# Optimization experiments

Measured on AMD Instinct MI355X. Metric: run time of the kernel, lower is better.

## Reference

```python
import jax, jax.numpy as jnp
import numpy as np

B, S, I, H = 64, 512, 512, 1024


def setup_inputs() -> dict:
    key = jax.random.key(0)
    ks = jax.random.split(key, 5)
    bound = 1.0 / np.sqrt(H)  # nn.GRUCell default init
    u = lambda k, shape: jax.random.uniform(k, shape, jnp.float32, -bound, bound)
    return {
        "input": jax.random.normal(ks[0], (B, S, I), jnp.float32),
        "state": jnp.zeros((B, H), jnp.float32),
        "weight_ih": u(ks[1], (3 * H, I)),
        "weight_hh": u(ks[2], (3 * H, H)),
        "bias_ih": u(ks[3], (3 * H,)),
        "bias_hh": u(ks[4], (3 * H,)),
        "gamma_ih": jnp.ones((3 * H,), jnp.float32),
        "gamma_hh": jnp.ones((3 * H,), jnp.float32),
    }


def _ln_x(x, g, b):
    # kefirski's _layer_norm_x: (x - mean) / std (unbiased std, eps=0)
    mean = jnp.mean(x, axis=-1, keepdims=True)
    std = jnp.std(x, axis=-1, keepdims=True, ddof=1)
    return g * ((x - mean) / std) + b


def _ln_h(x, g, b):
    # kefirski's _layer_norm_h: mean-subtraction only
    return g * (x - jnp.mean(x, axis=-1, keepdims=True)) + b


def reference(input, state, weight_ih, weight_hh, bias_ih, bias_hh, gamma_ih, gamma_hh):
    Hd = state.shape[-1]
    # Input-side projections + LN are h-independent -> precompute over all timesteps
    ih = jnp.einsum("bsi,gi->bsg", input, weight_ih)  # [B,S,3H]
    ih_rz = _ln_x(ih[..., : 2 * Hd], gamma_ih[: 2 * Hd], bias_ih[: 2 * Hd])  # [B,S,2H]
    ih_n = _ln_x(ih[..., 2 * Hd :], gamma_ih[2 * Hd :], bias_ih[2 * Hd :])  # [B,S,H]

    def step(h, xs):
        irz, inn = xs  # [B,2H], [B,H]
        hh = h @ weight_hh.T  # [B,3H]
        hh_rz = _ln_h(hh[:, : 2 * Hd], gamma_hh[: 2 * Hd], bias_hh[: 2 * Hd])
        hh_n = _ln_h(hh[:, 2 * Hd :], gamma_hh[2 * Hd :], bias_hh[2 * Hd :])
        rz = jax.nn.sigmoid(irz + hh_rz)
        r, z = rz[:, :Hd], rz[:, Hd:]
        n = jnp.tanh(inn + r * hh_n)
        h_new = (1.0 - z) * n + z * h
        return h_new, h_new

    final_state, outs = jax.lax.scan(
        step, state, (ih_rz.transpose(1, 0, 2), ih_n.transpose(1, 0, 2))
    )
    return outs.transpose(1, 0, 2), final_state  # [B,S,H], [B,H]
```

## Files before the change

### kernel.cpp

```cpp
#include <hip/hip_runtime.h>
#include <stdint.h>
#include <stddef.h>

#define B_  64
#define S_  512
#define I_  512
#define H_  1024
#define G_  3072
#define NWG 64
#define CPW 32

typedef short short8 __attribute__((ext_vector_type(8)));
typedef float f32x4  __attribute__((ext_vector_type(4)));
typedef unsigned short u16x4 __attribute__((ext_vector_type(4)));

__device__ __forceinline__ unsigned short f32_to_bf16(float f){
  unsigned u = __builtin_bit_cast(unsigned, f);
  u = (u + 0x7FFFu + ((u >> 16) & 1u)) >> 16;
  return (unsigned short)u;
}
__device__ __forceinline__ float bf16_to_f32(unsigned short s){
  unsigned u = ((unsigned)s) << 16;
  return __builtin_bit_cast(float, u);
}
__device__ __forceinline__ float sig_(float x){ return 1.0f/(1.0f + __expf(-x)); }
__device__ __forceinline__ float tanh_(float x){
  float ax = fabsf(x);
  float t = __expf(-2.0f*ax);
  float r = (1.0f - t)/(1.0f + t);
  return copysignf(r, x);
}

__device__ __forceinline__ short8 ldg16_coh(const unsigned short* p){
  short8 r;
  asm volatile("global_load_dwordx4 %0, %1, off sc0 sc1" : "=v"(r) : "v"(p) : "memory");
  return r;
}
__device__ __forceinline__ void stg8_coh(unsigned short* p, u16x4 v){
  asm volatile("global_store_dwordx2 %0, %1, off sc0 sc1" :: "v"(p), "v"(v) : "memory");
}
__device__ __forceinline__ void stg4_coh(unsigned* p, unsigned v){
  asm volatile("global_store_dword %0, %1, off sc0 sc1" :: "v"(p), "v"(v) : "memory");
}
__device__ __forceinline__ unsigned ldg4_coh_wait(const unsigned* p){
  unsigned r;
  asm volatile("global_load_dword %0, %1, off sc0 sc1\n\ts_waitcnt vmcnt(0)"
               : "=v"(r) : "v"(p) : "memory");
  return r;
}
__device__ __forceinline__ u16x4 ldg8(const unsigned short* p){
  u16x4 r;
  asm volatile("global_load_dwordx2 %0, %1, off" : "=v"(r) : "v"(p) : "memory");
  return r;
}

__global__ __launch_bounds__(256) void k_cvt4(const float* __restrict__ src,
                                              unsigned short* __restrict__ dst, int n4){
  int i = blockIdx.x*blockDim.x + threadIdx.x;
  int st = gridDim.x*blockDim.x;
  for (; i < n4; i += st){
    f32x4 v = *(const f32x4*)(src + (size_t)i*4);
    u16x4 o;
    o[0]=f32_to_bf16(v[0]); o[1]=f32_to_bf16(v[1]);
    o[2]=f32_to_bf16(v[2]); o[3]=f32_to_bf16(v[3]);
    *(u16x4*)(dst + (size_t)i*4) = o;
  }
}

__global__ __launch_bounds__(256) void k_cmean(const float* __restrict__ whh,
                                               unsigned short* __restrict__ CM){
  int k = blockIdx.x*256 + threadIdx.x;
  float s0 = 0.f, s1 = 0.f;
  for (int j = 0; j < 2048; ++j) s0 += whh[(size_t)j*H_ + k];
  for (int j = 2048; j < 3072; ++j) s1 += whh[(size_t)j*H_ + k];
  CM[k]      = f32_to_bf16(s0 * (1.0f/2048.0f));
  CM[H_ + k] = f32_to_bf16(s1 * (1.0f/1024.0f));
  for (int r = 2; r < 16; ++r) CM[(size_t)r*H_ + k] = 0;
}

__global__ __launch_bounds__(256, 2) void k_gemm_ih(
    const unsigned short* __restrict__ X,
    const unsigned short* __restrict__ W,
    unsigned short* __restrict__ IH)
{
  __shared__ __align__(16) short As[128*32];
  __shared__ __align__(16) short Bs[128*32];
  int bid = blockIdx.x;
  int mt = bid / 24, nt = bid % 24;
  int tid = threadIdx.x, lane = tid & 63, wid = tid >> 6;
  int vr = wid >> 1, vc = wid & 1;
  int r0s = tid >> 2, r1s = r0s + 64;
  int sc = (tid & 3) * 8;
  const unsigned short* xa0 = X + (size_t)(mt*128 + r0s)*512 + sc;
  const unsigned short* xa1 = X + (size_t)(mt*128 + r1s)*512 + sc;
  const unsigned short* wb0 = W + (size_t)(nt*128 + r0s)*512 + sc;
  const unsigned short* wb1 = W + (size_t)(nt*128 + r1s)*512 + sc;

  f32x4 acc[4][4];
  #pragma unroll
  for (int m=0;m<4;m++)
    #pragma unroll
    for (int n=0;n<4;n++) acc[m][n] = (f32x4){0.f,0.f,0.f,0.f};

  short8 ra0 = *(const short8*)xa0;
  short8 ra1 = *(const short8*)xa1;
  short8 rb0 = *(const short8*)wb0;
  short8 rb1 = *(const short8*)wb1;
  int ko = (lane >> 4) * 8;

  for (int kt = 0; kt < 16; ++kt){
    __syncthreads();
    *(short8*)&As[r0s*32 + sc] = ra0;
    *(short8*)&As[r1s*32 + sc] = ra1;
    *(short8*)&Bs[r0s*32 + sc] = rb0;
    *(short8*)&Bs[r1s*32 + sc] = rb1;
    __syncthreads();
    if (kt < 15){
      ra0 = *(const short8*)(xa0 + (kt+1)*32);
      ra1 = *(const short8*)(xa1 + (kt+1)*32);
      rb0 = *(const short8*)(wb0 + (kt+1)*32);
      rb1 = *(const short8*)(wb1 + (kt+1)*32);
    }
    short8 af[4], bfr[4];
    #pragma unroll
    for (int m=0;m<4;m++) af[m]  = *(const short8*)&As[(vr*64 + m*16 + (lane&15))*32 + ko];
    #pragma unroll
    for (int n=0;n<4;n++) bfr[n] = *(const short8*)&Bs[(vc*64 + n*16 + (lane&15))*32 + ko];
    #pragma unroll
    for (int m=0;m<4;m++)
      #pragma unroll
      for (int n=0;n<4;n++)
        acc[m][n] = __builtin_amdgcn_mfma_f32_16x16x32_bf16(af[m], bfr[n], acc[m][n], 0,0,0);
  }
  int row0 = mt*128 + vr*64, col0 = nt*128 + vc*64;
  int rl = (lane >> 4) * 4, cl = lane & 15;
  #pragma unroll
  for (int m=0;m<4;m++)
    #pragma unroll
    for (int n=0;n<4;n++)
      #pragma unroll
      for (int r=0;r<4;r++){
        int row = row0 + m*16 + rl + r;
        int rowT = ((row & 511) << 6) | (row >> 9);
        IH[(size_t)rowT*G_ + (col0 + n*16 + cl)] = f32_to_bf16(acc[m][n][r]);
      }
}

__global__ __launch_bounds__(256) void k_ln(
    unsigned short* __restrict__ IH,
    const float* __restrict__ gih,
    const float* __restrict__ bih)
{
  __shared__ float red[4][4];
  int row = blockIdx.x, tid = threadIdx.x, lane = tid & 63, wid = tid >> 6;
  unsigned short* p = IH + (size_t)row * G_;
  float xv[3][4];
  #pragma unroll
  for (int q=0;q<3;q++){
    u16x4 v = *(const u16x4*)(p + (tid + q*256)*4);
    #pragma unroll
    for (int j=0;j<4;j++) xv[q][j] = bf16_to_f32(v[j]);
  }
  float s0=0, q0=0, s1=0, q1=0;
  #pragma unroll
  for (int q=0;q<2;q++)
    #pragma unroll
    for (int j=0;j<4;j++){ s0 += xv[q][j]; q0 += xv[q][j]*xv[q][j]; }
  #pragma unroll
  for (int j=0;j<4;j++){ s1 += xv[2][j]; q1 += xv[2][j]*xv[2][j]; }
  #pragma unroll
  for (int off=32; off>0; off>>=1){
    s0 += __shfl_down(s0, off, 64);
    q0 += __shfl_down(q0, off, 64);
    s1 += __shfl_down(s1, off, 64);
    q1 += __shfl_down(q1, off, 64);
  }
  if (lane == 0){ red[wid][0]=s0; red[wid][1]=q0; red[wid][2]=s1; red[wid][3]=q1; }
  __syncthreads();
  float S0 = red[0][0]+red[1][0]+red[2][0]+red[3][0];
  float Q0 = red[0][1]+red[1][1]+red[2][1]+red[3][1];
  float S1 = red[0][2]+red[1][2]+red[2][2]+red[3][2];
  float Q1 = red[0][3]+red[1][3]+red[2][3]+red[3][3];
  float m0 = S0 * (1.0f/2048.0f);
  float rs0 = rsqrtf(fmaxf((Q0 - S0*m0) * (1.0f/2047.0f), 1e-20f));
  float m1 = S1 * (1.0f/1024.0f);
  float rs1 = rsqrtf(fmaxf((Q1 - S1*m1) * (1.0f/1023.0f), 1e-20f));
  #pragma unroll
  for (int q=0;q<3;q++){
    int base = (tid + q*256)*4;
    u16x4 o;
    #pragma unroll
    for (int j=0;j<4;j++){
      int col = base + j;
      float y = (q<2) ? (xv[q][j]-m0)*rs0 : (xv[q][j]-m1)*rs1;
      o[j] = f32_to_bf16(gih[col]*y + bih[col]);
    }
    *(u16x4*)(p + base) = o;
  }
}

__global__ __launch_bounds__(256, 1) void k_gru(
    const unsigned short* __restrict__ IH,
    const unsigned short* __restrict__ WHH,
    const unsigned short* __restrict__ CM,
    unsigned short* __restrict__ HB,
    const float* __restrict__ ghh,
    const float* __restrict__ bhh,
    const float* __restrict__ state,
    float* __restrict__ out,
    unsigned* __restrict__ FLAGS)
{
  __shared__ float PSUM[4][112][34];
  const int g = blockIdx.x & 31;
  const int p = blockIdx.x >> 5;
  const int tid = threadIdx.x;
  const int lane = tid & 63;
  const int wv = tid >> 6;
  const int l15 = lane & 15;
  const int lho = (lane >> 4) << 3;
  const int colbase = g * CPW;
  const int rowbase = p * 32;

  short8 bfr[7][8];
  #pragma unroll
  for (int ct = 0; ct < 7; ++ct){
    const unsigned short* src = (ct < 6)
        ? (WHH + (size_t)((ct>>1)*H_ + colbase + (ct&1)*16 + l15)*H_)
        : (CM + (size_t)l15*H_);
    #pragma unroll
    for (int ks = 0; ks < 8; ++ks)
      bfr[ct][ks] = *(const short8*)(src + wv*256 + ks*32 + lho);
  }

  const int b_ = tid & 31;
  const int cq = tid >> 5;
  const int c0 = colbase + cq*4;
  const int gb = rowbase + b_;
  float gr[4],gz[4],gn[4],br_[4],bz_[4],bn_[4],hv[4];
  #pragma unroll
  for (int j = 0; j < 4; ++j){
    gr[j] = ghh[c0+j];   gz[j] = ghh[H_+c0+j];   gn[j] = ghh[2*H_+c0+j];
    br_[j]= bhh[c0+j];   bz_[j]= bhh[H_+c0+j];   bn_[j]= bhh[2*H_+c0+j];
    hv[j] = state[(size_t)gb*H_ + c0 + j];
  }

  const unsigned* myflag = FLAGS + (p*32 + (lane & 31))*16;
  int cur = 0;

  for (int t = 0; t < S_; ++t){
    const unsigned short* ihp = IH + ((size_t)t*B_ + gb)*G_;
    u16x4 ir  = ldg8(ihp + c0);
    u16x4 izv = ldg8(ihp + H_ + c0);
    u16x4 inv = ldg8(ihp + 2*H_ + c0);

    for (;;){
      unsigned v = ldg4_coh_wait(myflag);
      if (__all((int)(v >= (unsigned)t))) break;
    }

    const unsigned short* hb = HB + cur*(B_*H_);
    short8 af[8][2];
    #pragma unroll
    for (int ks = 0; ks < 8; ++ks)
      #pragma unroll
      for (int rt = 0; rt < 2; ++rt)
        af[ks][rt] = ldg16_coh(hb + (size_t)(rowbase + rt*16 + l15)*H_ + wv*256 + ks*32 + lho);

    f32x4 acc[7][2];
    #pragma unroll
    for (int ct = 0; ct < 7; ++ct)
      #pragma unroll
      for (int rt = 0; rt < 2; ++rt)
        acc[ct][rt] = (f32x4){0.f,0.f,0.f,0.f};

    #pragma unroll
    for (int ks = 0; ks < 8; ++ks){
      asm volatile("s_waitcnt vmcnt(%0)" :: "i"(14 - 2*ks) : "memory");
      __builtin_amdgcn_sched_barrier(0);
      #pragma unroll
      for (int rt = 0; rt < 2; ++rt)
        #pragma unroll
        for (int ct = 0; ct < 7; ++ct)
          acc[ct][rt] = __builtin_amdgcn_mfma_f32_16x16x32_bf16(af[ks][rt], bfr[ct][ks], acc[ct][rt], 0,0,0);
    }

    #pragma unroll
    for (int ct = 0; ct < 7; ++ct)
      #pragma unroll
      for (int rt = 0; rt < 2; ++rt)
        *(f32x4*)&PSUM[wv][ct*16 + l15][rt*16 + (lane>>4)*4] = acc[ct][rt];
    __syncthreads();

    float hhr[4]={0,0,0,0}, hhz[4]={0,0,0,0}, hhn[4]={0,0,0,0};
    float mrz = 0.f, mn = 0.f;
    #pragma unroll
    for (int w = 0; w < 4; ++w){
      #pragma unroll
      for (int j = 0; j < 4; ++j){
        hhr[j] += PSUM[w][cq*4 + j][b_];
        hhz[j] += PSUM[w][32 + cq*4 + j][b_];
        hhn[j] += PSUM[w][64 + cq*4 + j][b_];
      }
      mrz += PSUM[w][96][b_];
      mn  += PSUM[w][97][b_];
    }
    f32x4 ho;
    #pragma unroll
    for (int j = 0; j < 4; ++j){
      float R = sig_(bf16_to_f32(ir[j])  + gr[j]*(hhr[j]-mrz) + br_[j]);
      float Z = sig_(bf16_to_f32(izv[j]) + gz[j]*(hhz[j]-mrz) + bz_[j]);
      float N = tanh_(bf16_to_f32(inv[j]) + R*(gn[j]*(hhn[j]-mn) + bn_[j]));
      hv[j] = (1.0f - Z)*N + Z*hv[j];
      ho[j] = hv[j];
    }
    u16x4 h16;
    #pragma unroll
    for (int j = 0; j < 4; ++j) h16[j] = f32_to_bf16(hv[j]);
    stg8_coh(HB + (cur^1)*(B_*H_) + (size_t)gb*H_ + c0, h16);

    asm volatile("s_waitcnt vmcnt(0)" ::: "memory");
    __syncthreads();
    if (tid == 0) stg4_coh((unsigned*)(FLAGS + (p*32 + g)*16), (unsigned)(t+1));
    *(f32x4*)(out + ((size_t)gb*S_ + t)*H_ + c0) = ho;
    cur ^= 1;
  }
  #pragma unroll
  for (int j = 0; j < 4; ++j)
    out[(size_t)B_*S_*H_ + (size_t)gb*H_ + c0 + j] = hv[j];
}

extern "C" void kernel_launch(void* const* d_in, const int* in_sizes, int n_in,
                              void* d_out, int out_size, void* d_ws, size_t ws_size,
                              hipStream_t stream){
  (void)in_sizes; (void)n_in; (void)out_size; (void)ws_size;
  const float* x   = (const float*)d_in[0];
  const float* st  = (const float*)d_in[1];
  const float* wih = (const float*)d_in[2];
  const float* whh = (const float*)d_in[3];
  const float* bih = (const float*)d_in[4];
  const float* bhh = (const float*)d_in[5];
  const float* gih = (const float*)d_in[6];
  const float* ghh = (const float*)d_in[7];
  float* out = (float*)d_out;
  char* ws = (char*)d_ws;

  unsigned short* IH    = (unsigned short*)(ws);
  unsigned short* X16   = (unsigned short*)(ws + 201326592ull);
  unsigned short* WIH16 = (unsigned short*)(ws + 234881024ull);
  unsigned short* WHH16 = (unsigned short*)(ws + 238026752ull);
  unsigned short* CM16  = (unsigned short*)(ws + 244318208ull);
  unsigned short* HB    = (unsigned short*)(ws + 244350976ull);
  unsigned*       FLAGS = (unsigned*)      (ws + 244613120ull);

  hipMemsetAsync(FLAGS, 0, 4096, stream);
  k_cvt4<<<2048, 256, 0, stream>>>(x,   X16,   4194304);
  k_cvt4<<<1024, 256, 0, stream>>>(wih, WIH16, 393216);
  k_cvt4<<<1024, 256, 0, stream>>>(whh, WHH16, 786432);
  k_cvt4<<<64,   256, 0, stream>>>(st,  HB,    16384);
  k_cmean<<<4,   256, 0, stream>>>(whh, CM16);
  k_gemm_ih<<<6144, 256, 0, stream>>>(X16, WIH16, IH);
  k_ln<<<32768, 256, 0, stream>>>(IH, gih, bih);
  k_gru<<<NWG, 256, 0, stream>>>(IH, WHH16, CM16, HB, ghh, bhh, st, out, FLAGS);
}
```

Baseline: 3.052 ms.

## Halve GRU workgroups and split each step into four independently-flagged batch groups

The recurrent kernel now launches 32 workgroups, one per 32-column strip, and each walks all 64 batch rows as four sequential groups of 16. Each group has its own completion flag per strip, so a group can start its next timestep as soon as that group is finished in every strip. The aim is to pipeline the cross-workgroup synchronisation across batch groups and use fewer workgroups. The cost is that each workgroup now runs four serial load, barrier and store rounds per timestep with smaller MFMA batches, so latency per step may grow.

Measured after the change: 7.550 ms. 147% more time.

```diff
diff --git a/kernel.cpp b/kernel.cpp
--- a/kernel.cpp
+++ b/kernel.cpp
@@ -7,11 +7,13 @@
 #define I_  512
 #define H_  1024
 #define G_  3072
-#define NWG 64
+#define NWG 32
 #define CPW 32
+#define NGRP 4
 
 typedef short short8 __attribute__((ext_vector_type(8)));
 typedef float f32x4  __attribute__((ext_vector_type(4)));
+typedef float f32x2  __attribute__((ext_vector_type(2)));
 typedef unsigned short u16x4 __attribute__((ext_vector_type(4)));
 
 __device__ __forceinline__ unsigned short f32_to_bf16(float f){
@@ -36,9 +38,6 @@
   asm volatile("global_load_dwordx4 %0, %1, off sc0 sc1" : "=v"(r) : "v"(p) : "memory");
   return r;
 }
-__device__ __forceinline__ void stg8_coh(unsigned short* p, u16x4 v){
-  asm volatile("global_store_dwordx2 %0, %1, off sc0 sc1" :: "v"(p), "v"(v) : "memory");
-}
 __device__ __forceinline__ void stg4_coh(unsigned* p, unsigned v){
   asm volatile("global_store_dword %0, %1, off sc0 sc1" :: "v"(p), "v"(v) : "memory");
 }
@@ -48,9 +47,9 @@
                : "=v"(r) : "v"(p) : "memory");
   return r;
 }
-__device__ __forceinline__ u16x4 ldg8(const unsigned short* p){
-  u16x4 r;
-  asm volatile("global_load_dwordx2 %0, %1, off" : "=v"(r) : "v"(p) : "memory");
+__device__ __forceinline__ unsigned ldg4p(const unsigned short* p){
+  unsigned r;
+  asm volatile("global_load_dword %0, %1, off" : "=v"(r) : "v"(p) : "memory");
   return r;
 }
 
@@ -210,16 +209,14 @@
     float* __restrict__ out,
     unsigned* __restrict__ FLAGS)
 {
-  __shared__ float PSUM[4][112][34];
-  const int g = blockIdx.x & 31;
-  const int p = blockIdx.x >> 5;
+  __shared__ float PSUM[4][112][18];
+  const int strip = blockIdx.x;
   const int tid = threadIdx.x;
   const int lane = tid & 63;
   const int wv = tid >> 6;
   const int l15 = lane & 15;
   const int lho = (lane >> 4) << 3;
-  const int colbase = g * CPW;
-  const int rowbase = p * 32;
+  const int colbase = strip * CPW;
 
   short8 bfr[7][8];
   #pragma unroll
@@ -232,101 +229,100 @@
       bfr[ct][ks] = *(const short8*)(src + wv*256 + ks*32 + lho);
   }
 
-  const int b_ = tid & 31;
-  const int cq = tid >> 5;
-  const int c0 = colbase + cq*4;
-  const int gb = rowbase + b_;
-  float gr[4],gz[4],gn[4],br_[4],bz_[4],bn_[4],hv[4];
-  #pragma unroll
-  for (int j = 0; j < 4; ++j){
-    gr[j] = ghh[c0+j];   gz[j] = ghh[H_+c0+j];   gn[j] = ghh[2*H_+c0+j];
-    br_[j]= bhh[c0+j];   bz_[j]= bhh[H_+c0+j];   bn_[j]= bhh[2*H_+c0+j];
-    hv[j] = state[(size_t)gb*H_ + c0 + j];
-  }
-
-  const unsigned* myflag = FLAGS + (p*32 + (lane & 31))*16;
-  int cur = 0;
+  const int b_ = tid & 15;
+  const int cp = tid >> 4;
+  const int c0 = colbase + 2*cp;
+  float gr[2],gz[2],gn[2],br_[2],bz_[2],bn_[2];
+  #pragma unroll
+  for (int j = 0; j < 2; ++j){
+    int col = c0 + j;
+    gr[j] = ghh[col];  gz[j] = ghh[H_+col];  gn[j] = ghh[2*H_+col];
+    br_[j]= bhh[col];  bz_[j]= bhh[H_+col];  bn_[j]= bhh[2*H_+col];
+  }
+  float hv[NGRP][2];
+  #pragma unroll
+  for (int g = 0; g < NGRP; ++g)
+    #pragma unroll
+    for (int j = 0; j < 2; ++j)
+      hv[g][j] = state[(size_t)(g*16 + b_)*H_ + c0 + j];
 
   for (int t = 0; t < S_; ++t){
-    const unsigned short* ihp = IH + ((size_t)t*B_ + gb)*G_;
-    u16x4 ir  = ldg8(ihp + c0);
-    u16x4 izv = ldg8(ihp + H_ + c0);
-    u16x4 inv = ldg8(ihp + 2*H_ + c0);
-
-    for (;;){
-      unsigned v = ldg4_coh_wait(myflag);
-      if (__all((int)(v >= (unsigned)t))) break;
-    }
-
-    const unsigned short* hb = HB + cur*(B_*H_);
-    short8 af[8][2];
-    #pragma unroll
-    for (int ks = 0; ks < 8; ++ks)
-      #pragma unroll
-      for (int rt = 0; rt < 2; ++rt)
-        af[ks][rt] = ldg16_coh(hb + (size_t)(rowbase + rt*16 + l15)*H_ + wv*256 + ks*32 + lho);
-
-    f32x4 acc[7][2];
-    #pragma unroll
-    for (int ct = 0; ct < 7; ++ct)
-      #pragma unroll
-      for (int rt = 0; rt < 2; ++rt)
-        acc[ct][rt] = (f32x4){0.f,0.f,0.f,0.f};
-
-    #pragma unroll
-    for (int ks = 0; ks < 8; ++ks){
-      asm volatile("s_waitcnt vmcnt(%0)" :: "i"(14 - 2*ks) : "memory");
-      __builtin_amdgcn_sched_barrier(0);
-      #pragma unroll
-      for (int rt = 0; rt < 2; ++rt)
+    const unsigned short* hbR = HB + (t & 1)*(B_*H_);
+    unsigned short*       hbW = (unsigned short*)HB + ((t+1) & 1)*(B_*H_);
+    #pragma unroll
+    for (int g = 0; g < NGRP; ++g){
+      const int gb = g*16 + b_;
+      const unsigned short* ihp = IH + ((size_t)t*B_ + gb)*G_;
+      unsigned irv = ldg4p(ihp + c0);
+      unsigned izv = ldg4p(ihp + H_ + c0);
+      unsigned inv = ldg4p(ihp + 2*H_ + c0);
+
+      const unsigned* myflag = FLAGS + (size_t)(g*32 + (lane & 31))*16;
+      for (;;){
+        unsigned v = ldg4_coh_wait(myflag);
+        if (__all((int)(v >= (unsigned)t))) break;
+      }
+
+      short8 af[8];
+      #pragma unroll
+      for (int ks = 0; ks < 8; ++ks)
+        af[ks] = ldg16_coh(hbR + (size_t)(g*16 + l15)*H_ + wv*256 + ks*32 + lho);
+
+      f32x4 acc[7];
+      #pragma unroll
+      for (int ct = 0; ct < 7; ++ct) acc[ct] = (f32x4){0.f,0.f,0.f,0.f};
+      #pragma unroll
+      for (int ks = 0; ks < 8; ++ks){
+        asm volatile("s_waitcnt vmcnt(%0)" :: "i"(7-ks) : "memory");
+        __builtin_amdgcn_sched_barrier(0);
         #pragma unroll
         for (int ct = 0; ct < 7; ++ct)
-          acc[ct][rt] = __builtin_amdgcn_mfma_f32_16x16x32_bf16(af[ks][rt], bfr[ct][ks], acc[ct][rt], 0,0,0);
+          acc[ct] = __builtin_amdgcn_mfma_f32_16x16x32_bf16(af[ks], bfr[ct][ks], acc[ct], 0,0,0);
+      }
+
+      #pragma unroll
+      for (int ct = 0; ct < 7; ++ct)
+        *(f32x4*)&PSUM[wv][ct*16 + l15][(lane>>4)*4] = acc[ct];
+      __syncthreads();
+
+      float hr[2]={0,0}, hz[2]={0,0}, hn[2]={0,0};
+      float mrz = 0.f, mn = 0.f;
+      #pragma unroll
+      for (int w = 0; w < 4; ++w){
+        #pragma unroll
+        for (int j = 0; j < 2; ++j){
+          int cl = 2*cp + j, half = cl >> 4, idx = cl & 15;
+          hr[j] += PSUM[w][half*16 + idx][b_];
+          hz[j] += PSUM[w][32 + half*16 + idx][b_];
+          hn[j] += PSUM[w][64 + half*16 + idx][b_];
+        }
+        mrz += PSUM[w][96][b_];
+        mn  += PSUM[w][97][b_];
+      }
+      f32x2 ho;
+      unsigned hpack = 0;
+      #pragma unroll
+      for (int j = 0; j < 2; ++j){
+        float R = sig_(bf16_to_f32((unsigned short)(j ? (irv>>16) : irv)) + gr[j]*(hr[j]-mrz) + br_[j]);
+        float Z = sig_(bf16_to_f32((unsigned short)(j ? (izv>>16) : izv)) + gz[j]*(hz[j]-mrz) + bz_[j]);
+        float N = tanh_(bf16_to_f32((unsigned short)(j ? (inv>>16) : inv)) + R*(gn[j]*(hn[j]-mn) + bn_[j]));
+        hv[g][j] = (1.0f - Z)*N + Z*hv[g][j];
+        ho[j] = hv[g][j];
+        hpack |= ((unsigned)f32_to_bf16(hv[g][j])) << (16*j);
+      }
+      stg4_coh((unsigned*)(hbW + (size_t)gb*H_ + c0), hpack);
+
+      asm volatile("s_waitcnt vmcnt(0)" ::: "memory");
+      __syncthreads();
+      if (tid == 0) stg4_coh(FLAGS + (size_t)(g*32 + strip)*16, (unsigned)(t+1));
+      *(f32x2*)(out + ((size_t)gb*S_ + t)*H_ + c0) = ho;
     }
-
-    #pragma unroll
-    for (int ct = 0; ct < 7; ++ct)
-      #pragma unroll
-      for (int rt = 0; rt < 2; ++rt)
-        *(f32x4*)&PSUM[wv][ct*16 + l15][rt*16 + (lane>>4)*4] = acc[ct][rt];
-    __syncthreads();
-
-    float hhr[4]={0,0,0,0}, hhz[4]={0,0,0,0}, hhn[4]={0,0,0,0};
-    float mrz = 0.f, mn = 0.f;
-    #pragma unroll
-    for (int w = 0; w < 4; ++w){
-      #pragma unroll
-      for (int j = 0; j < 4; ++j){
-        hhr[j] += PSUM[w][cq*4 + j][b_];
-        hhz[j] += PSUM[w][32 + cq*4 + j][b_];
-        hhn[j] += PSUM[w][64 + cq*4 + j][b_];
-      }
-      mrz += PSUM[w][96][b_];
-      mn  += PSUM[w][97][b_];
-    }
-    f32x4 ho;
-    #pragma unroll
-    for (int j = 0; j < 4; ++j){
-      float R = sig_(bf16_to_f32(ir[j])  + gr[j]*(hhr[j]-mrz) + br_[j]);
-      float Z = sig_(bf16_to_f32(izv[j]) + gz[j]*(hhz[j]-mrz) + bz_[j]);
-      float N = tanh_(bf16_to_f32(inv[j]) + R*(gn[j]*(hhn[j]-mn) + bn_[j]));
-      hv[j] = (1.0f - Z)*N + Z*hv[j];
-      ho[j] = hv[j];
-    }
-    u16x4 h16;
-    #pragma unroll
-    for (int j = 0; j < 4; ++j) h16[j] = f32_to_bf16(hv[j]);
-    stg8_coh(HB + (cur^1)*(B_*H_) + (size_t)gb*H_ + c0, h16);
-
-    asm volatile("s_waitcnt vmcnt(0)" ::: "memory");
-    __syncthreads();
-    if (tid == 0) stg4_coh((unsigned*)(FLAGS + (p*32 + g)*16), (unsigned)(t+1));
-    *(f32x4*)(out + ((size_t)gb*S_ + t)*H_ + c0) = ho;
-    cur ^= 1;
-  }
-  #pragma unroll
-  for (int j = 0; j < 4; ++j)
-    out[(size_t)B_*S_*H_ + (size_t)gb*H_ + c0 + j] = hv[j];
+  }
+  #pragma unroll
+  for (int g = 0; g < NGRP; ++g)
+    #pragma unroll
+    for (int j = 0; j < 2; ++j)
+      out[(size_t)B_*S_*H_ + (size_t)(g*16 + b_)*H_ + c0 + j] = hv[g][j];
 }
 
 extern "C" void kernel_launch(void* const* d_in, const int* in_sizes, int n_in,
@@ -352,7 +348,7 @@
   unsigned short* HB    = (unsigned short*)(ws + 244350976ull);
   unsigned*       FLAGS = (unsigned*)      (ws + 244613120ull);
 
-  hipMemsetAsync(FLAGS, 0, 4096, stream);
+  hipMemsetAsync(FLAGS, 0, 8192, stream);
   k_cvt4<<<2048, 256, 0, stream>>>(x,   X16,   4194304);
   k_cvt4<<<1024, 256, 0, stream>>>(wih, WIH16, 393216);
   k_cvt4<<<1024, 256, 0, stream>>>(whh, WHH16, 786432);
```

## Replace flag-based inter-block sync with parity-tagged bf16 hidden-state polling

Applied to the files above, without the earlier changes.

Removes the per-step flag store/poll handshake between workgroups and instead embeds a step-parity tag in the low mantissa bit of each bf16 hidden value, so consumers spin on the hidden-state data itself until all tags match the expected phase. Gate math is also reorganized so only half the threads (128) compute 8 columns each with 16-byte loads/stores. This is meant to cut a round-trip of global-memory latency per timestep from the serial recurrence. In exchange it perturbs the hidden state's rounding by one bf16 ulp, re-reads the full A tile on every failed poll, and leaves half the threads idle during the elementwise phase.

Result: slower. 4.463 ms (+46.2%).

```diff
diff --git a/kernel.cpp b/kernel.cpp
--- a/kernel.cpp
+++ b/kernel.cpp
@@ -13,6 +13,7 @@
 typedef short short8 __attribute__((ext_vector_type(8)));
 typedef float f32x4  __attribute__((ext_vector_type(4)));
 typedef unsigned short u16x4 __attribute__((ext_vector_type(4)));
+typedef unsigned uint4v __attribute__((ext_vector_type(4)));
 
 __device__ __forceinline__ unsigned short f32_to_bf16(float f){
   unsigned u = __builtin_bit_cast(unsigned, f);
@@ -22,6 +23,15 @@
 __device__ __forceinline__ float bf16_to_f32(unsigned short s){
   unsigned u = ((unsigned)s) << 16;
   return __builtin_bit_cast(float, u);
+}
+__device__ __forceinline__ unsigned short bf16_tag(float f, unsigned tag){
+  unsigned short t16 = f32_to_bf16(f);
+  if (((unsigned)t16 & 1u) != tag){
+    unsigned short a = (unsigned short)(t16 - 1), b = (unsigned short)(t16 + 1);
+    float fa = bf16_to_f32(a), fb = bf16_to_f32(b);
+    t16 = (fabsf(fa - f) <= fabsf(fb - f)) ? a : b;
+  }
+  return t16;
 }
 __device__ __forceinline__ float sig_(float x){ return 1.0f/(1.0f + __expf(-x)); }
 __device__ __forceinline__ float tanh_(float x){
@@ -36,21 +46,12 @@
   asm volatile("global_load_dwordx4 %0, %1, off sc0 sc1" : "=v"(r) : "v"(p) : "memory");
   return r;
 }
-__device__ __forceinline__ void stg8_coh(unsigned short* p, u16x4 v){
-  asm volatile("global_store_dwordx2 %0, %1, off sc0 sc1" :: "v"(p), "v"(v) : "memory");
-}
-__device__ __forceinline__ void stg4_coh(unsigned* p, unsigned v){
-  asm volatile("global_store_dword %0, %1, off sc0 sc1" :: "v"(p), "v"(v) : "memory");
-}
-__device__ __forceinline__ unsigned ldg4_coh_wait(const unsigned* p){
-  unsigned r;
-  asm volatile("global_load_dword %0, %1, off sc0 sc1\n\ts_waitcnt vmcnt(0)"
-               : "=v"(r) : "v"(p) : "memory");
-  return r;
-}
-__device__ __forceinline__ u16x4 ldg8(const unsigned short* p){
-  u16x4 r;
-  asm volatile("global_load_dwordx2 %0, %1, off" : "=v"(r) : "v"(p) : "memory");
+__device__ __forceinline__ void stg16_coh(unsigned short* p, uint4v v){
+  asm volatile("global_store_dwordx4 %0, %1, off sc0 sc1" :: "v"(p), "v"(v) : "memory");
+}
+__device__ __forceinline__ short8 ldg16p(const unsigned short* p){
+  short8 r;
+  asm volatile("global_load_dwordx4 %0, %1, off" : "=v"(r) : "v"(p) : "memory");
   return r;
 }
 
@@ -64,6 +65,18 @@
     o[0]=f32_to_bf16(v[0]); o[1]=f32_to_bf16(v[1]);
     o[2]=f32_to_bf16(v[2]); o[3]=f32_to_bf16(v[3]);
     *(u16x4*)(dst + (size_t)i*4) = o;
+  }
+}
+
+__global__ __launch_bounds__(256) void k_cvt_state(const float* __restrict__ st,
+                                                   unsigned short* __restrict__ HB){
+  int i = (blockIdx.x*256 + threadIdx.x)*4;
+  #pragma unroll
+  for (int j = 0; j < 4; ++j){
+    float v = st[i+j];
+    unsigned short b0 = bf16_tag(v, 0u);
+    HB[i+j] = b0;
+    HB[B_*H_ + i + j] = (unsigned short)(b0 | 1u);
   }
 }
 
@@ -207,8 +220,7 @@
     const float* __restrict__ ghh,
     const float* __restrict__ bhh,
     const float* __restrict__ state,
-    float* __restrict__ out,
-    unsigned* __restrict__ FLAGS)
+    float* __restrict__ out)
 {
   __shared__ float PSUM[4][112][34];
   const int g = blockIdx.x & 31;
@@ -233,38 +245,55 @@
   }
 
   const int b_ = tid & 31;
-  const int cq = tid >> 5;
-  const int c0 = colbase + cq*4;
+  const int oc = (tid >> 5) & 3;
+  const bool gateT = (tid < 128);
+  const int c0 = colbase + oc*8;
   const int gb = rowbase + b_;
-  float gr[4],gz[4],gn[4],br_[4],bz_[4],bn_[4],hv[4];
-  #pragma unroll
-  for (int j = 0; j < 4; ++j){
-    gr[j] = ghh[c0+j];   gz[j] = ghh[H_+c0+j];   gn[j] = ghh[2*H_+c0+j];
-    br_[j]= bhh[c0+j];   bz_[j]= bhh[H_+c0+j];   bn_[j]= bhh[2*H_+c0+j];
-    hv[j] = state[(size_t)gb*H_ + c0 + j];
-  }
-
-  const unsigned* myflag = FLAGS + (p*32 + (lane & 31))*16;
-  int cur = 0;
+  float gr[8],gz[8],gn[8],br_[8],bz_[8],bn_[8],hv[8];
+  if (gateT){
+    #pragma unroll
+    for (int j = 0; j < 8; ++j){
+      int col = c0 + j;
+      gr[j] = ghh[col];  gz[j] = ghh[H_+col];  gn[j] = ghh[2*H_+col];
+      br_[j]= bhh[col];  bz_[j]= bhh[H_+col];  bn_[j]= bhh[2*H_+col];
+      hv[j] = state[(size_t)gb*H_ + col];
+    }
+  }
 
   for (int t = 0; t < S_; ++t){
-    const unsigned short* ihp = IH + ((size_t)t*B_ + gb)*G_;
-    u16x4 ir  = ldg8(ihp + c0);
-    u16x4 izv = ldg8(ihp + H_ + c0);
-    u16x4 inv = ldg8(ihp + 2*H_ + c0);
-
+    const unsigned tagR = (unsigned)((t >> 1) & 1);
+    const unsigned expw = tagR * 0x00010001u;
+    const unsigned tagW = (unsigned)(((t+1) >> 1) & 1);
+    const unsigned short* hbR = HB + (t & 1)*(B_*H_);
+    unsigned short*       hbW = (unsigned short*)HB + ((t+1) & 1)*(B_*H_);
+
+    short8 ihr, ihz, ihn;
+    if (gateT){
+      const unsigned short* ihp = IH + ((size_t)t*B_ + gb)*G_;
+      ihr = ldg16p(ihp + c0);
+      ihz = ldg16p(ihp + H_ + c0);
+      ihn = ldg16p(ihp + 2*H_ + c0);
+    }
+
+    short8 af[8][2];
     for (;;){
-      unsigned v = ldg4_coh_wait(myflag);
-      if (__all((int)(v >= (unsigned)t))) break;
-    }
-
-    const unsigned short* hb = HB + cur*(B_*H_);
-    short8 af[8][2];
-    #pragma unroll
-    for (int ks = 0; ks < 8; ++ks)
-      #pragma unroll
-      for (int rt = 0; rt < 2; ++rt)
-        af[ks][rt] = ldg16_coh(hb + (size_t)(rowbase + rt*16 + l15)*H_ + wv*256 + ks*32 + lho);
+      #pragma unroll
+      for (int ks = 0; ks < 8; ++ks)
+        #pragma unroll
+        for (int rt = 0; rt < 2; ++rt)
+          af[ks][rt] = ldg16_coh(hbR + (size_t)(rowbase + rt*16 + l15)*H_ + wv*256 + ks*32 + lho);
+      asm volatile("s_waitcnt vmcnt(0)" ::: "memory");
+      unsigned bad = 0;
+      #pragma unroll
+      for (int ks = 0; ks < 8; ++ks)
+        #pragma unroll
+        for (int rt = 0; rt < 2; ++rt){
+          uint4v d = __builtin_bit_cast(uint4v, af[ks][rt]);
+          #pragma unroll
+          for (int q = 0; q < 4; ++q) bad |= (d[q] ^ expw) & 0x00010001u;
+        }
+      if (__all(bad == 0)) break;
+    }
 
     f32x4 acc[7][2];
     #pragma unroll
@@ -272,17 +301,13 @@
       #pragma unroll
       for (int rt = 0; rt < 2; ++rt)
         acc[ct][rt] = (f32x4){0.f,0.f,0.f,0.f};
-
-    #pragma unroll
-    for (int ks = 0; ks < 8; ++ks){
-      asm volatile("s_waitcnt vmcnt(%0)" :: "i"(14 - 2*ks) : "memory");
-      __builtin_amdgcn_sched_barrier(0);
+    #pragma unroll
+    for (int ks = 0; ks < 8; ++ks)
       #pragma unroll
       for (int rt = 0; rt < 2; ++rt)
         #pragma unroll
         for (int ct = 0; ct < 7; ++ct)
           acc[ct][rt] = __builtin_amdgcn_mfma_f32_16x16x32_bf16(af[ks][rt], bfr[ct][ks], acc[ct][rt], 0,0,0);
-    }
 
     #pragma unroll
     for (int ct = 0; ct < 7; ++ct)
@@ -291,42 +316,50 @@
         *(f32x4*)&PSUM[wv][ct*16 + l15][rt*16 + (lane>>4)*4] = acc[ct][rt];
     __syncthreads();
 
-    float hhr[4]={0,0,0,0}, hhz[4]={0,0,0,0}, hhn[4]={0,0,0,0};
-    float mrz = 0.f, mn = 0.f;
-    #pragma unroll
-    for (int w = 0; w < 4; ++w){
-      #pragma unroll
-      for (int j = 0; j < 4; ++j){
-        hhr[j] += PSUM[w][cq*4 + j][b_];
-        hhz[j] += PSUM[w][32 + cq*4 + j][b_];
-        hhn[j] += PSUM[w][64 + cq*4 + j][b_];
+    if (gateT){
+      float hr[8], hz[8], hn[8];
+      float mrz = 0.f, mn = 0.f;
+      #pragma unroll
+      for (int j = 0; j < 8; ++j){ hr[j]=0.f; hz[j]=0.f; hn[j]=0.f; }
+      #pragma unroll
+      for (int w = 0; w < 4; ++w){
+        #pragma unroll
+        for (int j = 0; j < 8; ++j){
+          int cl = oc*8 + j;
+          hr[j] += PSUM[w][cl][b_];
+          hz[j] += PSUM[w][32 + cl][b_];
+          hn[j] += PSUM[w][64 + cl][b_];
+        }
+        mrz += PSUM[w][96][b_];
+        mn  += PSUM[w][97][b_];
       }
-      mrz += PSUM[w][96][b_];
-      mn  += PSUM[w][97][b_];
-    }
-    f32x4 ho;
-    #pragma unroll
-    for (int j = 0; j < 4; ++j){
-      float R = sig_(bf16_to_f32(ir[j])  + gr[j]*(hhr[j]-mrz) + br_[j]);
-      float Z = sig_(bf16_to_f32(izv[j]) + gz[j]*(hhz[j]-mrz) + bz_[j]);
-      float N = tanh_(bf16_to_f32(inv[j]) + R*(gn[j]*(hhn[j]-mn) + bn_[j]));
-      hv[j] = (1.0f - Z)*N + Z*hv[j];
-      ho[j] = hv[j];
-    }
-    u16x4 h16;
-    #pragma unroll
-    for (int j = 0; j < 4; ++j) h16[j] = f32_to_bf16(hv[j]);
-    stg8_coh(HB + (cur^1)*(B_*H_) + (size_t)gb*H_ + c0, h16);
-
-    asm volatile("s_waitcnt vmcnt(0)" ::: "memory");
+      f32x4 ho0, ho1;
+      unsigned short hp[8];
+      #pragma unroll
+      for (int j = 0; j < 8; ++j){
+        float R = sig_(bf16_to_f32((unsigned short)ihr[j]) + gr[j]*(hr[j]-mrz) + br_[j]);
+        float Z = sig_(bf16_to_f32((unsigned short)ihz[j]) + gz[j]*(hz[j]-mrz) + bz_[j]);
+        float N = tanh_(bf16_to_f32((unsigned short)ihn[j]) + R*(gn[j]*(hn[j]-mn) + bn_[j]));
+        hv[j] = (1.0f - Z)*N + Z*hv[j];
+        if (j < 4) ho0[j] = hv[j]; else ho1[j-4] = hv[j];
+        hp[j] = bf16_tag(hv[j], tagW);
+      }
+      float* op = out + ((size_t)gb*S_ + t)*H_ + c0;
+      *(f32x4*)op       = ho0;
+      *(f32x4*)(op + 4) = ho1;
+      uint4v pk;
+      #pragma unroll
+      for (int q = 0; q < 4; ++q)
+        pk[q] = (unsigned)hp[2*q] | ((unsigned)hp[2*q+1] << 16);
+      stg16_coh(hbW + (size_t)gb*H_ + c0, pk);
+    }
     __syncthreads();
-    if (tid == 0) stg4_coh((unsigned*)(FLAGS + (p*32 + g)*16), (unsigned)(t+1));
-    *(f32x4*)(out + ((size_t)gb*S_ + t)*H_ + c0) = ho;
-    cur ^= 1;
-  }
-  #pragma unroll
-  for (int j = 0; j < 4; ++j)
-    out[(size_t)B_*S_*H_ + (size_t)gb*H_ + c0 + j] = hv[j];
+  }
+  if (gateT){
+    #pragma unroll
+    for (int j = 0; j < 8; ++j)
+      out[(size_t)B_*S_*H_ + (size_t)gb*H_ + c0 + j] = hv[j];
+  }
 }
 
 extern "C" void kernel_launch(void* const* d_in, const int* in_sizes, int n_in,
@@ -350,15 +383,13 @@
   unsigned short* WHH16 = (unsigned short*)(ws + 238026752ull);
   unsigned short* CM16  = (unsigned short*)(ws + 244318208ull);
   unsigned short* HB    = (unsigned short*)(ws + 244350976ull);
-  unsigned*       FLAGS = (unsigned*)      (ws + 244613120ull);
-
-  hipMemsetAsync(FLAGS, 0, 4096, stream);
+
   k_cvt4<<<2048, 256, 0, stream>>>(x,   X16,   4194304);
   k_cvt4<<<1024, 256, 0, stream>>>(wih, WIH16, 393216);
   k_cvt4<<<1024, 256, 0, stream>>>(whh, WHH16, 786432);
-  k_cvt4<<<64,   256, 0, stream>>>(st,  HB,    16384);
+  k_cvt_state<<<64, 256, 0, stream>>>(st, HB);
   k_cmean<<<4,   256, 0, stream>>>(whh, CM16);
   k_gemm_ih<<<6144, 256, 0, stream>>>(X16, WIH16, IH);
   k_ln<<<32768, 256, 0, stream>>>(IH, gih, bih);
-  k_gru<<<NWG, 256, 0, stream>>>(IH, WHH16, CM16, HB, ghh, bhh, st, out, FLAGS);
-}
+  k_gru<<<NWG, 256, 0, stream>>>(IH, WHH16, CM16, HB, ghh, bhh, st, out);
+}
```

## Replace flag-based inter-block sync with parity-tagged bf16 hidden-state data

Applied to the files above, without the earlier changes.

Removes the per-step flag store/poll handshake between workgroups. Each bf16 hidden value now carries a parity tag in its low mantissa bit, and readers spin-load the hidden-state tiles until every element shows the expected tag. This drops the flag round trip and the vmcnt(0) drain before signaling. In exchange the rounding of h is slightly perturbed, and the MFMA pipelining that overlapped loads with compute is lost because all loads now complete before any compute starts.

Result: slower. 3.722 ms (+21.9%).

```diff
diff --git a/kernel.cpp b/kernel.cpp
--- a/kernel.cpp
+++ b/kernel.cpp
@@ -13,6 +13,7 @@
 typedef short short8 __attribute__((ext_vector_type(8)));
 typedef float f32x4  __attribute__((ext_vector_type(4)));
 typedef unsigned short u16x4 __attribute__((ext_vector_type(4)));
+typedef unsigned uint4v __attribute__((ext_vector_type(4)));
 
 __device__ __forceinline__ unsigned short f32_to_bf16(float f){
   unsigned u = __builtin_bit_cast(unsigned, f);
@@ -22,6 +23,15 @@
 __device__ __forceinline__ float bf16_to_f32(unsigned short s){
   unsigned u = ((unsigned)s) << 16;
   return __builtin_bit_cast(float, u);
+}
+__device__ __forceinline__ unsigned short bf16_tag(float f, unsigned tag){
+  unsigned short t16 = f32_to_bf16(f);
+  if (((unsigned)t16 & 1u) != tag){
+    unsigned short a = (unsigned short)(t16 - 1), b = (unsigned short)(t16 + 1);
+    float fa = bf16_to_f32(a), fb = bf16_to_f32(b);
+    t16 = (fabsf(fa - f) <= fabsf(fb - f)) ? a : b;
+  }
+  return t16;
 }
 __device__ __forceinline__ float sig_(float x){ return 1.0f/(1.0f + __expf(-x)); }
 __device__ __forceinline__ float tanh_(float x){
@@ -38,15 +48,6 @@
 }
 __device__ __forceinline__ void stg8_coh(unsigned short* p, u16x4 v){
   asm volatile("global_store_dwordx2 %0, %1, off sc0 sc1" :: "v"(p), "v"(v) : "memory");
-}
-__device__ __forceinline__ void stg4_coh(unsigned* p, unsigned v){
-  asm volatile("global_store_dword %0, %1, off sc0 sc1" :: "v"(p), "v"(v) : "memory");
-}
-__device__ __forceinline__ unsigned ldg4_coh_wait(const unsigned* p){
-  unsigned r;
-  asm volatile("global_load_dword %0, %1, off sc0 sc1\n\ts_waitcnt vmcnt(0)"
-               : "=v"(r) : "v"(p) : "memory");
-  return r;
 }
 __device__ __forceinline__ u16x4 ldg8(const unsigned short* p){
   u16x4 r;
@@ -64,6 +65,18 @@
     o[0]=f32_to_bf16(v[0]); o[1]=f32_to_bf16(v[1]);
     o[2]=f32_to_bf16(v[2]); o[3]=f32_to_bf16(v[3]);
     *(u16x4*)(dst + (size_t)i*4) = o;
+  }
+}
+
+__global__ __launch_bounds__(256) void k_cvt_state(const float* __restrict__ st,
+                                                   unsigned short* __restrict__ HB){
+  int i = (blockIdx.x*256 + threadIdx.x)*4;
+  #pragma unroll
+  for (int j = 0; j < 4; ++j){
+    float v = st[i+j];
+    unsigned short b0 = bf16_tag(v, 0u);
+    HB[i+j] = b0;
+    HB[B_*H_ + i + j] = (unsigned short)(b0 | 1u);
   }
 }
 
@@ -207,8 +220,7 @@
     const float* __restrict__ ghh,
     const float* __restrict__ bhh,
     const float* __restrict__ state,
-    float* __restrict__ out,
-    unsigned* __restrict__ FLAGS)
+    float* __restrict__ out)
 {
   __shared__ float PSUM[4][112][34];
   const int g = blockIdx.x & 31;
@@ -244,27 +256,43 @@
     hv[j] = state[(size_t)gb*H_ + c0 + j];
   }
 
-  const unsigned* myflag = FLAGS + (p*32 + (lane & 31))*16;
-  int cur = 0;
-
   for (int t = 0; t < S_; ++t){
+    const unsigned tagR = (unsigned)((t >> 1) & 1);
+    const unsigned expw = tagR * 0x00010001u;
+    const unsigned tagW = (unsigned)(((t+1) >> 1) & 1);
+    const unsigned short* hbR = HB + (t & 1)*(B_*H_);
+    unsigned short*       hbW = (unsigned short*)HB + ((t+1) & 1)*(B_*H_);
+
     const unsigned short* ihp = IH + ((size_t)t*B_ + gb)*G_;
     u16x4 ir  = ldg8(ihp + c0);
     u16x4 izv = ldg8(ihp + H_ + c0);
     u16x4 inv = ldg8(ihp + 2*H_ + c0);
 
-    for (;;){
-      unsigned v = ldg4_coh_wait(myflag);
-      if (__all((int)(v >= (unsigned)t))) break;
-    }
-
-    const unsigned short* hb = HB + cur*(B_*H_);
     short8 af[8][2];
-    #pragma unroll
-    for (int ks = 0; ks < 8; ++ks)
-      #pragma unroll
-      for (int rt = 0; rt < 2; ++rt)
-        af[ks][rt] = ldg16_coh(hb + (size_t)(rowbase + rt*16 + l15)*H_ + wv*256 + ks*32 + lho);
+    unsigned pend = 0xFFFFu;
+    do {
+      #pragma unroll
+      for (int ks = 0; ks < 8; ++ks)
+        #pragma unroll
+        for (int rt = 0; rt < 2; ++rt)
+          if (pend & (1u << (ks*2 + rt)))
+            af[ks][rt] = ldg16_coh(hbR + (size_t)(rowbase + rt*16 + l15)*H_ + wv*256 + ks*32 + lho);
+      asm volatile("s_waitcnt vmcnt(0)" ::: "memory");
+      #pragma unroll
+      for (int ks = 0; ks < 8; ++ks)
+        #pragma unroll
+        for (int rt = 0; rt < 2; ++rt){
+          unsigned bit = 1u << (ks*2 + rt);
+          if (pend & bit){
+            uint4v d = __builtin_bit_cast(uint4v, af[ks][rt]);
+            unsigned bad = 0;
+            #pragma unroll
+            for (int q = 0; q < 4; ++q) bad |= (d[q] ^ expw) & 0x00010001u;
+            if (__all(bad == 0)) pend &= ~bit;
+          }
+        }
+      pend = __builtin_amdgcn_readfirstlane(pend);
+    } while (pend);
 
     f32x4 acc[7][2];
     #pragma unroll
@@ -272,17 +300,13 @@
       #pragma unroll
       for (int rt = 0; rt < 2; ++rt)
         acc[ct][rt] = (f32x4){0.f,0.f,0.f,0.f};
-
-    #pragma unroll
-    for (int ks = 0; ks < 8; ++ks){
-      asm volatile("s_waitcnt vmcnt(%0)" :: "i"(14 - 2*ks) : "memory");
-      __builtin_amdgcn_sched_barrier(0);
+    #pragma unroll
+    for (int ks = 0; ks < 8; ++ks)
       #pragma unroll
       for (int rt = 0; rt < 2; ++rt)
         #pragma unroll
         for (int ct = 0; ct < 7; ++ct)
           acc[ct][rt] = __builtin_amdgcn_mfma_f32_16x16x32_bf16(af[ks][rt], bfr[ct][ks], acc[ct][rt], 0,0,0);
-    }
 
     #pragma unroll
     for (int ct = 0; ct < 7; ++ct)
@@ -305,6 +329,7 @@
       mn  += PSUM[w][97][b_];
     }
     f32x4 ho;
+    u16x4 h16;
     #pragma unroll
     for (int j = 0; j < 4; ++j){
       float R = sig_(bf16_to_f32(ir[j])  + gr[j]*(hhr[j]-mrz) + br_[j]);
@@ -312,17 +337,11 @@
       float N = tanh_(bf16_to_f32(inv[j]) + R*(gn[j]*(hhn[j]-mn) + bn_[j]));
       hv[j] = (1.0f - Z)*N + Z*hv[j];
       ho[j] = hv[j];
+      h16[j] = bf16_tag(hv[j], tagW);
     }
-    u16x4 h16;
-    #pragma unroll
-    for (int j = 0; j < 4; ++j) h16[j] = f32_to_bf16(hv[j]);
-    stg8_coh(HB + (cur^1)*(B_*H_) + (size_t)gb*H_ + c0, h16);
-
-    asm volatile("s_waitcnt vmcnt(0)" ::: "memory");
+    stg8_coh(hbW + (size_t)gb*H_ + c0, h16);
+    *(f32x4*)(out + ((size_t)gb*S_ + t)*H_ + c0) = ho;
     __syncthreads();
-    if (tid == 0) stg4_coh((unsigned*)(FLAGS + (p*32 + g)*16), (unsigned)(t+1));
-    *(f32x4*)(out + ((size_t)gb*S_ + t)*H_ + c0) = ho;
-    cur ^= 1;
   }
   #pragma unroll
   for (int j = 0; j < 4; ++j)
@@ -350,15 +369,13 @@
   unsigned short* WHH16 = (unsigned short*)(ws + 238026752ull);
   unsigned short* CM16  = (unsigned short*)(ws + 244318208ull);
   unsigned short* HB    = (unsigned short*)(ws + 244350976ull);
-  unsigned*       FLAGS = (unsigned*)      (ws + 244613120ull);
-
-  hipMemsetAsync(FLAGS, 0, 4096, stream);
+
   k_cvt4<<<2048, 256, 0, stream>>>(x,   X16,   4194304);
   k_cvt4<<<1024, 256, 0, stream>>>(wih, WIH16, 393216);
   k_cvt4<<<1024, 256, 0, stream>>>(whh, WHH16, 786432);
-  k_cvt4<<<64,   256, 0, stream>>>(st,  HB,    16384);
+  k_cvt_state<<<64, 256, 0, stream>>>(st, HB);
   k_cmean<<<4,   256, 0, stream>>>(whh, CM16);
   k_gemm_ih<<<6144, 256, 0, stream>>>(X16, WIH16, IH);
   k_ln<<<32768, 256, 0, stream>>>(IH, gih, bih);
-  k_gru<<<NWG, 256, 0, stream>>>(IH, WHH16, CM16, HB, ghh, bhh, st, out, FLAGS);
-}
+  k_gru<<<NWG, 256, 0, stream>>>(IH, WHH16, CM16, HB, ghh, bhh, st, out);
+}
```
